# Performance work log

Measured on AMD Instinct MI355X. Metric: run time of the kernel, lower is better.

## Reference

```python
import jax, jax.numpy as jnp
import numpy as np

INPUT_SIZE = 16
HIDDEN = 256


def setup_inputs() -> dict:
    key = jax.random.key(0)
    ks = jax.random.split(key, 12)
    B, T, F, H = 512, 168, INPUT_SIZE, HIDDEN
    s_ih = 1.0 / np.sqrt(H)
    def u(k, shape):
        return jax.random.uniform(k, shape, jnp.float32, -s_ih, s_ih)
    return {
        "x": jax.random.normal(ks[0], (B, T, F), jnp.float32),
        # LSTM params, torch gate order (i, f, g, o) stacked along dim 0
        "w_ih": u(ks[1], (4 * H, F)),
        "w_hh": u(ks[2], (4 * H, H)),
        "b_ih": u(ks[3], (4 * H,)),
        "b_hh": u(ks[4], (4 * H,)),
        # MLP params
        "fc1_w": u(ks[5], (128, H)),
        "fc1_b": u(ks[6], (128,)),
        "fc2_w": u(ks[7], (64, 128)),
        "fc2_b": u(ks[8], (64,)),
        "fc3_w": u(ks[9], (1, 64)),
        "fc3_b": u(ks[10], (1,)),
    }


def _lstm(x, w_ih, w_hh, b_ih, b_hh):
    B, T, F = x.shape
    H = w_hh.shape[1]
    # Precompute input contribution for all timesteps: [B, T, 4H]
    x_proj = jnp.einsum("btf,gf->btg", x, w_ih) + b_ih + b_hh

    def step(carry, xp_t):
        h, c = carry
        gates = xp_t + h @ w_hh.T  # [B, 4H]
        i, f, g, o = jnp.split(gates, 4, axis=-1)
        i = jax.nn.sigmoid(i)
        f = jax.nn.sigmoid(f)
        g = jnp.tanh(g)
        o = jax.nn.sigmoid(o)
        c = f * c + i * g
        h = o * jnp.tanh(c)
        return (h, c), h

    h0 = jnp.zeros((B, H), x.dtype)
    c0 = jnp.zeros((B, H), x.dtype)
    (_, _), hs = jax.lax.scan(step, (h0, c0), jnp.swapaxes(x_proj, 0, 1))
    return jnp.swapaxes(hs, 0, 1)  # [B, T, H]


def reference(x, w_ih, w_hh, b_ih, b_hh, fc1_w, fc1_b, fc2_w, fc2_b, fc3_w, fc3_b):
    h = _lstm(x, w_ih, w_hh, b_ih, b_hh)          # [B, T, H]
    h = jax.nn.relu(h @ fc1_w.T + fc1_b)           # [B, T, 128]
    h = jax.nn.relu(h @ fc2_w.T + fc2_b)           # [B, T, 64]
    out = h @ fc3_w.T + fc3_b                      # [B, T, 1]
    return out
```

## Files before the change

### kernel.cpp

```cpp
#include <hip/hip_runtime.h>

typedef _Float16 half8 __attribute__((ext_vector_type(8)));
typedef float floatx4 __attribute__((ext_vector_type(4)));
typedef unsigned uint4v __attribute__((ext_vector_type(4)));

#define Bsz 512
#define Tsz 168
#define Fsz 16
#define Hsz 256
#define KTILES 9
#define LDS_K 296

#define WSW_OFF   0
#define BIAS_OFF  589824
#define HH_OFF    675840
#define XBUF_OFF  (HH_OFF + 44040192)

__global__ __launch_bounds__(256) void k_prep(
    const float* __restrict__ w_hh, const float* __restrict__ w_ih,
    const float* __restrict__ b_ih, const float* __restrict__ b_hh,
    _Float16* __restrict__ wsw, float* __restrict__ bias) {
    const int b = blockIdx.x, tid = threadIdx.x;
    const int lane = tid & 63, sub = tid >> 6;
    if (b < 144) {
        int tile = b * 4 + sub;
        int nt = tile / KTILES, kt = tile - nt * KTILES;
        int n_in = lane & 15, kg = lane >> 4;
        int J = nt >> 2, g = nt & 3;
        int n_orig = g * 256 + J * 16 + n_in;
        half8 v;
#pragma unroll
        for (int e = 0; e < 8; ++e) {
            int k = kt * 32 + kg * 8 + e;
            float f;
            if (k < 256)      f = w_hh[n_orig * 256 + k];
            else if (k < 272) f = w_ih[n_orig * 16 + (k - 256)];
            else              f = 0.0f;
            v[e] = (_Float16)f;
        }
        ((half8*)wsw)[tile * 64 + lane] = v;
    } else {
        int id = (b - 144) * 256 + tid;
        int nt = id >> 4, n = id & 15;
        int J = nt >> 2, g = nt & 3;
        int n_orig = g * 256 + J * 16 + n;
        bias[id] = b_ih[n_orig] + b_hh[n_orig];
    }
}

#define WG_BARRIER()                                          \
    do {                                                      \
        asm volatile("s_waitcnt lgkmcnt(0)" ::: "memory");    \
        __builtin_amdgcn_s_barrier();                         \
        __builtin_amdgcn_sched_barrier(0);                    \
    } while (0)

__global__ __launch_bounds__(512, 1) void k_lstm21(
    const float* __restrict__ x, const _Float16* __restrict__ wsw,
    const float* __restrict__ bias, unsigned* __restrict__ hh32,
    unsigned long long* __restrict__ xbuf) {
    __shared__ __align__(16) _Float16 h_lds[16][LDS_K];
    __shared__ float glds[4][16][68];

    const int tid = threadIdx.x;
    const int wave = tid >> 6, lane = tid & 63;
    const int n_in = lane & 15, quad = lane >> 4;
    const int bb = blockIdx.x & 31, ng = blockIdx.x >> 5;
    const int b0 = bb * 16;
    const int Jl = wave & 3;
    const int gp = wave >> 2;

    float bs[2];
    half8 wf[2][KTILES];
#pragma unroll
    for (int gg = 0; gg < 2; ++gg) {
        const int nt = ng * 16 + Jl * 4 + gp * 2 + gg;
        bs[gg] = bias[nt * 16 + n_in];
#pragma unroll
        for (int kt = 0; kt < KTILES; ++kt)
            wf[gg][kt] = ((const half8*)wsw)[((size_t)nt * KTILES + kt) * 64 + lane];
    }

    for (int i = tid; i < 16 * LDS_K; i += 512)
        ((_Float16*)h_lds)[i] = (_Float16)0.0f;
    __syncthreads();
    if (tid < 256) {
        int m = tid >> 4, f = tid & 15;
        h_lds[m][Hsz + f] = (_Float16)x[((b0 + m) * Tsz + 0) * Fsz + f];
    }
    __syncthreads();

    const int cm = tid >> 5, cj = tid & 31;
    float c_st[2] = {0.f, 0.f};

    for (int t = 0; t < Tsz; ++t) {
        half8 afr[KTILES];
#pragma unroll
        for (int kt = 0; kt < KTILES; ++kt)
            afr[kt] = *(const half8*)&h_lds[n_in][kt * 32 + quad * 8];

        floatx4 acc[2] = {(floatx4){0.f,0.f,0.f,0.f}, (floatx4){0.f,0.f,0.f,0.f}};
#pragma unroll
        for (int gg = 0; gg < 2; ++gg) {
#pragma unroll
            for (int kt = 0; kt < KTILES; ++kt)
                acc[gg] = __builtin_amdgcn_mfma_f32_16x16x32_f16(afr[kt], wf[gg][kt], acc[gg], 0, 0, 0);
        }

#pragma unroll
        for (int gg = 0; gg < 2; ++gg)
#pragma unroll
            for (int r = 0; r < 4; ++r)
                glds[gp * 2 + gg][quad * 4 + r][Jl * 16 + n_in] = acc[gg][r] + bs[gg];
        WG_BARRIER();

        union { _Float16 f[2]; unsigned u; } pk;
#pragma unroll
        for (int e = 0; e < 2; ++e) {
            int jl = 2 * cj + e;
            float ig = glds[0][cm][jl];
            float fg = glds[1][cm][jl];
            float gg_ = glds[2][cm][jl];
            float og = glds[3][cm][jl];
            float si = 1.0f / (1.0f + __expf(-ig));
            float sf = 1.0f / (1.0f + __expf(-fg));
            float tg = 1.0f - 2.0f / (__expf(2.0f * gg_) + 1.0f);
            float so = 1.0f / (1.0f + __expf(-og));
            float c = sf * c_st[e] + si * tg;
            c_st[e] = c;
            float th = 1.0f - 2.0f / (__expf(2.0f * c) + 1.0f);
            pk.f[e] = (_Float16)(so * th);
        }
        *(unsigned*)&h_lds[cm][ng * 64 + 2 * cj] = pk.u;

        const size_t rb = ((size_t)((bb * 2 + (t & 1)) * 16));
        if (t + 1 < Tsz) {
            unsigned long long pv = ((unsigned long long)pk.u << 32) | (unsigned)(t + 1);
            __hip_atomic_store(&xbuf[(rb + cm) * 128 + ng * 32 + cj], pv,
                               __ATOMIC_RELAXED, __HIP_MEMORY_SCOPE_AGENT);
        }
        __builtin_nontemporal_store(
            pk.u, &hh32[((size_t)(b0 + cm) * Tsz + t) * 128 + ng * 32 + cj]);

        if (t + 1 < Tsz) {
            float xr = 0.0f;
            if (tid < 256)
                xr = x[((b0 + (tid >> 4)) * Tsz + (t + 1)) * Fsz + (tid & 15)];

            const unsigned want = (unsigned)(t + 1);
            unsigned long long* p1 = &xbuf[(rb + cm) * 128 + ((ng + 1) & 3) * 32 + cj];
            unsigned long long* p2 = &xbuf[(rb + cm) * 128 + ((ng + 2) & 3) * 32 + cj];
            unsigned long long* p3 = &xbuf[(rb + cm) * 128 + ((ng + 3) & 3) * 32 + cj];
            unsigned long long v1 = __hip_atomic_load(p1, __ATOMIC_RELAXED,
                                                      __HIP_MEMORY_SCOPE_AGENT);
            unsigned long long v2 = __hip_atomic_load(p2, __ATOMIC_RELAXED,
                                                      __HIP_MEMORY_SCOPE_AGENT);
            unsigned long long v3 = __hip_atomic_load(p3, __ATOMIC_RELAXED,
                                                      __HIP_MEMORY_SCOPE_AGENT);
            while ((unsigned)v1 != want || (unsigned)v2 != want || (unsigned)v3 != want) {
                if ((unsigned)v1 != want)
                    v1 = __hip_atomic_load(p1, __ATOMIC_RELAXED, __HIP_MEMORY_SCOPE_AGENT);
                if ((unsigned)v2 != want)
                    v2 = __hip_atomic_load(p2, __ATOMIC_RELAXED, __HIP_MEMORY_SCOPE_AGENT);
                if ((unsigned)v3 != want)
                    v3 = __hip_atomic_load(p3, __ATOMIC_RELAXED, __HIP_MEMORY_SCOPE_AGENT);
            }
            *(unsigned*)&h_lds[cm][((ng + 1) & 3) * 64 + 2 * cj] = (unsigned)(v1 >> 32);
            *(unsigned*)&h_lds[cm][((ng + 2) & 3) * 64 + 2 * cj] = (unsigned)(v2 >> 32);
            *(unsigned*)&h_lds[cm][((ng + 3) & 3) * 64 + 2 * cj] = (unsigned)(v3 >> 32);
            if (tid < 256)
                h_lds[tid >> 4][Hsz + (tid & 15)] = (_Float16)xr;
            WG_BARRIER();
        }
    }
}

__global__ __launch_bounds__(512, 2) void k_mlp7(
    const _Float16* __restrict__ hh, const float* __restrict__ fc1_w,
    const float* __restrict__ fc2_w, const float* __restrict__ b1,
    const float* __restrict__ b2, const float* __restrict__ w3,
    const float* __restrict__ b3, float* __restrict__ out) {
    __shared__ __align__(16) _Float16 w1sh[64 * 512];
    __shared__ __align__(16) _Float16 w2sh[16 * 512];
    __shared__ _Float16 st1[8][16][136];
    __shared__ _Float16 st2[8][16][72];

    const int tid = threadIdx.x;
    const int wave = tid >> 6, lane = tid & 63;
    const int n_in = lane & 15, quad = lane >> 4;

    {
#pragma unroll
        for (int it = 0; it < 8; ++it) {
            int s = it * 512 + tid;
            int tile = s >> 6, ln = s & 63;
            int nt = tile >> 3, kt = tile & 7, ni = ln & 15, kg = ln >> 4;
            const float* src = &fc1_w[(nt * 16 + ni) * 256 + kt * 32 + kg * 8];
            half8 v;
#pragma unroll
            for (int e = 0; e < 8; ++e) v[e] = (_Float16)src[e];
            ((half8*)w1sh)[s] = v;
        }
#pragma unroll
        for (int it = 0; it < 2; ++it) {
            int s = it * 512 + tid;
            int tile = s >> 6, ln = s & 63;
            int nt = tile >> 2, kt = tile & 3, ni = ln & 15, kg = ln >> 4;
            const float* src = &fc2_w[(nt * 16 + ni) * 128 + kt * 32 + kg * 8];
            half8 v;
#pragma unroll
            for (int e = 0; e < 8; ++e) v[e] = (_Float16)src[e];
            ((half8*)w2sh)[s] = v;
        }
    }
    __syncthreads();

    uint4v bufA[8], bufB[8], bufC[8];
    const int ch0 = blockIdx.x, ch1 = blockIdx.x + 224, ch2 = blockIdx.x + 448;

#define MLP_LOAD(dst, ch)                                                      \
    {                                                                          \
        const int tok0_ = (ch) * 128 + wave * 16;                              \
        _Pragma("unroll")                                                      \
        for (int kt = 0; kt < 8; ++kt)                                         \
            dst[kt] = *(const uint4v*)&hh[(size_t)(tok0_ + n_in) * 256 +       \
                                          kt * 32 + quad * 8];                 \
    }

    MLP_LOAD(bufA, ch0)
    MLP_LOAD(bufB, ch1)
    MLP_LOAD(bufC, ch2)

    auto compute = [&](const uint4v* raw, int chunk) {
        const int tok0 = chunk * 128 + wave * 16;
        half8 afr[8];
#pragma unroll
        for (int kt = 0; kt < 8; ++kt)
            afr[kt] = __builtin_bit_cast(half8, raw[kt]);

#pragma unroll
        for (int nt = 0; nt < 8; ++nt) {
            floatx4 a = (floatx4){0.f, 0.f, 0.f, 0.f};
#pragma unroll
            for (int kt = 0; kt < 8; ++kt) {
                half8 bfr = *(const half8*)&w1sh[(nt * 8 + kt) * 512 + lane * 8];
                a = __builtin_amdgcn_mfma_f32_16x16x32_f16(afr[kt], bfr, a, 0, 0, 0);
            }
            float bbv = b1[nt * 16 + n_in];
#pragma unroll
            for (int r = 0; r < 4; ++r) {
                float v = a[r] + bbv;
                st1[wave][quad * 4 + r][nt * 16 + n_in] = (_Float16)(v > 0.f ? v : 0.f);
            }
        }

        half8 a2[4];
#pragma unroll
        for (int kt = 0; kt < 4; ++kt)
            a2[kt] = *(const half8*)&st1[wave][n_in][kt * 32 + quad * 8];
#pragma unroll
        for (int nt = 0; nt < 4; ++nt) {
            floatx4 a = (floatx4){0.f, 0.f, 0.f, 0.f};
#pragma unroll
            for (int kt = 0; kt < 4; ++kt) {
                half8 bfr = *(const half8*)&w2sh[(nt * 4 + kt) * 512 + lane * 8];
                a = __builtin_amdgcn_mfma_f32_16x16x32_f16(a2[kt], bfr, a, 0, 0, 0);
            }
            float bbv = b2[nt * 16 + n_in];
#pragma unroll
            for (int r = 0; r < 4; ++r) {
                float v = a[r] + bbv;
                st2[wave][quad * 4 + r][nt * 16 + n_in] = (_Float16)(v > 0.f ? v : 0.f);
            }
        }

        float p = 0.0f;
#pragma unroll
        for (int e = 0; e < 16; ++e)
            p += (float)st2[wave][n_in][quad * 16 + e] * w3[quad * 16 + e];
        p += __shfl_down(p, 32);
        p += __shfl_down(p, 16);
        if (quad == 0) out[tok0 + n_in] = p + b3[0];
    };

    compute(bufA, ch0);
    compute(bufB, ch1);
    compute(bufC, ch2);
#undef MLP_LOAD
}

extern "C" void kernel_launch(void* const* d_in, const int* in_sizes, int n_in,
                              void* d_out, int out_size, void* d_ws, size_t ws_size,
                              hipStream_t stream) {
    const float* x     = (const float*)d_in[0];
    const float* w_ih  = (const float*)d_in[1];
    const float* w_hh  = (const float*)d_in[2];
    const float* b_ih  = (const float*)d_in[3];
    const float* b_hh  = (const float*)d_in[4];
    const float* fc1_w = (const float*)d_in[5];
    const float* fc1_b = (const float*)d_in[6];
    const float* fc2_w = (const float*)d_in[7];
    const float* fc2_b = (const float*)d_in[8];
    const float* fc3_w = (const float*)d_in[9];
    const float* fc3_b = (const float*)d_in[10];

    char* ws = (char*)d_ws;
    _Float16* wsw  = (_Float16*)(ws + WSW_OFF);
    float*    bias = (float*)(ws + BIAS_OFF);
    _Float16* hhist= (_Float16*)(ws + HH_OFF);
    unsigned long long* xbuf = (unsigned long long*)(ws + XBUF_OFF);

    k_prep<<<148, 256, 0, stream>>>(w_hh, w_ih, b_ih, b_hh, wsw, bias);
    k_lstm21<<<128, 512, 0, stream>>>(x, wsw, bias, (unsigned*)hhist, xbuf);
    k_mlp7<<<224, 512, 0, stream>>>(hhist, fc1_w, fc2_w, fc1_b, fc2_b,
                                    fc3_w, fc3_b, (float*)d_out);
}
```

Before: 431.1 us.

## Overlap cross-block h exchange with local-slice MFMAs in LSTM recurrence

Each step now first runs the MFMAs over the block's own h slice and the x tile, then waits for the other three blocks' h slices, and only then finishes the remaining K tiles. The spin-wait on the exchange buffer moves to the start of the next step, with the first atomic loads issued at the end of the previous step, and the x row is prefetched one step ahead. Only 6 of the 18 weight fragments stay in registers. The other 12 are reloaded from global/L2 every step, which adds memory traffic inside the critical loop in exchange for lower register pressure and more overlap.

```diff
diff --git a/kernel.cpp b/kernel.cpp
--- a/kernel.cpp
+++ b/kernel.cpp
@@ -55,7 +55,7 @@
         __builtin_amdgcn_sched_barrier(0);                    \
     } while (0)
 
-__global__ __launch_bounds__(512, 1) void k_lstm21(
+__global__ __launch_bounds__(512, 1) void k_lstm22(
     const float* __restrict__ x, const _Float16* __restrict__ wsw,
     const float* __restrict__ bias, unsigned* __restrict__ hh32,
     unsigned long long* __restrict__ xbuf) {
@@ -70,16 +70,20 @@
     const int Jl = wave & 3;
     const int gp = wave >> 2;
 
+    const int nt0 = ng * 16 + Jl * 4 + gp * 2 + 0;
+    const int nt1 = ng * 16 + Jl * 4 + gp * 2 + 1;
+    const int kt_o0 = 2 * ng, kt_o1 = 2 * ng + 1;
+
     float bs[2];
-    half8 wf[2][KTILES];
-#pragma unroll
-    for (int gg = 0; gg < 2; ++gg) {
-        const int nt = ng * 16 + Jl * 4 + gp * 2 + gg;
-        bs[gg] = bias[nt * 16 + n_in];
-#pragma unroll
-        for (int kt = 0; kt < KTILES; ++kt)
-            wf[gg][kt] = ((const half8*)wsw)[((size_t)nt * KTILES + kt) * 64 + lane];
-    }
+    bs[0] = bias[nt0 * 16 + n_in];
+    bs[1] = bias[nt1 * 16 + n_in];
+    const half8* wsw8 = (const half8*)wsw;
+    half8 w0o0 = wsw8[((size_t)nt0 * KTILES + kt_o0) * 64 + lane];
+    half8 w0o1 = wsw8[((size_t)nt0 * KTILES + kt_o1) * 64 + lane];
+    half8 w0x  = wsw8[((size_t)nt0 * KTILES + 8) * 64 + lane];
+    half8 w1o0 = wsw8[((size_t)nt1 * KTILES + kt_o0) * 64 + lane];
+    half8 w1o1 = wsw8[((size_t)nt1 * KTILES + kt_o1) * 64 + lane];
+    half8 w1x  = wsw8[((size_t)nt1 * KTILES + 8) * 64 + lane];
 
     for (int i = tid; i < 16 * LDS_K; i += 512)
         ((_Float16*)h_lds)[i] = (_Float16)0.0f;
@@ -92,19 +96,53 @@
 
     const int cm = tid >> 5, cj = tid & 31;
     float c_st[2] = {0.f, 0.f};
+    unsigned long long pv1 = 0, pv2 = 0, pv3 = 0;
+    float xr_a = 0.f, xr_b = 0.f;
+    if (tid < 256 && 1 < Tsz)
+        xr_a = x[((b0 + (tid >> 4)) * Tsz + 1) * Fsz + (tid & 15)];
 
     for (int t = 0; t < Tsz; ++t) {
-        half8 afr[KTILES];
-#pragma unroll
-        for (int kt = 0; kt < KTILES; ++kt)
-            afr[kt] = *(const half8*)&h_lds[n_in][kt * 32 + quad * 8];
-
         floatx4 acc[2] = {(floatx4){0.f,0.f,0.f,0.f}, (floatx4){0.f,0.f,0.f,0.f}};
-#pragma unroll
-        for (int gg = 0; gg < 2; ++gg) {
-#pragma unroll
-            for (int kt = 0; kt < KTILES; ++kt)
-                acc[gg] = __builtin_amdgcn_mfma_f32_16x16x32_f16(afr[kt], wf[gg][kt], acc[gg], 0, 0, 0);
+        {
+            half8 a0 = *(const half8*)&h_lds[n_in][kt_o0 * 32 + quad * 8];
+            half8 a1 = *(const half8*)&h_lds[n_in][kt_o1 * 32 + quad * 8];
+            half8 ax = *(const half8*)&h_lds[n_in][8 * 32 + quad * 8];
+            acc[0] = __builtin_amdgcn_mfma_f32_16x16x32_f16(a0, w0o0, acc[0], 0, 0, 0);
+            acc[1] = __builtin_amdgcn_mfma_f32_16x16x32_f16(a0, w1o0, acc[1], 0, 0, 0);
+            acc[0] = __builtin_amdgcn_mfma_f32_16x16x32_f16(a1, w0o1, acc[0], 0, 0, 0);
+            acc[1] = __builtin_amdgcn_mfma_f32_16x16x32_f16(a1, w1o1, acc[1], 0, 0, 0);
+            acc[0] = __builtin_amdgcn_mfma_f32_16x16x32_f16(ax, w0x, acc[0], 0, 0, 0);
+            acc[1] = __builtin_amdgcn_mfma_f32_16x16x32_f16(ax, w1x, acc[1], 0, 0, 0);
+        }
+
+        if (t > 0) {
+            const unsigned want = (unsigned)t;
+            const size_t rbp = (size_t)((bb * 2 + ((t + 1) & 1)) * 16);
+            unsigned long long* p1 = &xbuf[(rbp + cm) * 128 + ((ng + 1) & 3) * 32 + cj];
+            unsigned long long* p2 = &xbuf[(rbp + cm) * 128 + ((ng + 2) & 3) * 32 + cj];
+            unsigned long long* p3 = &xbuf[(rbp + cm) * 128 + ((ng + 3) & 3) * 32 + cj];
+            while ((unsigned)pv1 != want || (unsigned)pv2 != want || (unsigned)pv3 != want) {
+                if ((unsigned)pv1 != want)
+                    pv1 = __hip_atomic_load(p1, __ATOMIC_RELAXED, __HIP_MEMORY_SCOPE_AGENT);
+                if ((unsigned)pv2 != want)
+                    pv2 = __hip_atomic_load(p2, __ATOMIC_RELAXED, __HIP_MEMORY_SCOPE_AGENT);
+                if ((unsigned)pv3 != want)
+                    pv3 = __hip_atomic_load(p3, __ATOMIC_RELAXED, __HIP_MEMORY_SCOPE_AGENT);
+            }
+            *(unsigned*)&h_lds[cm][((ng + 1) & 3) * 64 + 2 * cj] = (unsigned)(pv1 >> 32);
+            *(unsigned*)&h_lds[cm][((ng + 2) & 3) * 64 + 2 * cj] = (unsigned)(pv2 >> 32);
+            *(unsigned*)&h_lds[cm][((ng + 3) & 3) * 64 + 2 * cj] = (unsigned)(pv3 >> 32);
+        }
+        WG_BARRIER();
+
+#pragma unroll
+        for (int i = 0; i < 6; ++i) {
+            const int kt = (kt_o0 + 2 + i) & 7;
+            half8 a  = *(const half8*)&h_lds[n_in][kt * 32 + quad * 8];
+            half8 wA = wsw8[((size_t)nt0 * KTILES + kt) * 64 + lane];
+            half8 wB = wsw8[((size_t)nt1 * KTILES + kt) * 64 + lane];
+            acc[0] = __builtin_amdgcn_mfma_f32_16x16x32_f16(a, wA, acc[0], 0, 0, 0);
+            acc[1] = __builtin_amdgcn_mfma_f32_16x16x32_f16(a, wB, acc[1], 0, 0, 0);
         }
 
 #pragma unroll
@@ -143,34 +181,19 @@
             pk.u, &hh32[((size_t)(b0 + cm) * Tsz + t) * 128 + ng * 32 + cj]);
 
         if (t + 1 < Tsz) {
-            float xr = 0.0f;
+            pv1 = __hip_atomic_load(&xbuf[(rb + cm) * 128 + ((ng + 1) & 3) * 32 + cj],
+                                    __ATOMIC_RELAXED, __HIP_MEMORY_SCOPE_AGENT);
+            pv2 = __hip_atomic_load(&xbuf[(rb + cm) * 128 + ((ng + 2) & 3) * 32 + cj],
+                                    __ATOMIC_RELAXED, __HIP_MEMORY_SCOPE_AGENT);
+            pv3 = __hip_atomic_load(&xbuf[(rb + cm) * 128 + ((ng + 3) & 3) * 32 + cj],
+                                    __ATOMIC_RELAXED, __HIP_MEMORY_SCOPE_AGENT);
+            if (t + 2 < Tsz && tid < 256)
+                xr_b = x[((b0 + (tid >> 4)) * Tsz + (t + 2)) * Fsz + (tid & 15)];
+
             if (tid < 256)
-                xr = x[((b0 + (tid >> 4)) * Tsz + (t + 1)) * Fsz + (tid & 15)];
-
-            const unsigned want = (unsigned)(t + 1);
-            unsigned long long* p1 = &xbuf[(rb + cm) * 128 + ((ng + 1) & 3) * 32 + cj];
-            unsigned long long* p2 = &xbuf[(rb + cm) * 128 + ((ng + 2) & 3) * 32 + cj];
-            unsigned long long* p3 = &xbuf[(rb + cm) * 128 + ((ng + 3) & 3) * 32 + cj];
-            unsigned long long v1 = __hip_atomic_load(p1, __ATOMIC_RELAXED,
-                                                      __HIP_MEMORY_SCOPE_AGENT);
-            unsigned long long v2 = __hip_atomic_load(p2, __ATOMIC_RELAXED,
-                                                      __HIP_MEMORY_SCOPE_AGENT);
-            unsigned long long v3 = __hip_atomic_load(p3, __ATOMIC_RELAXED,
-                                                      __HIP_MEMORY_SCOPE_AGENT);
-            while ((unsigned)v1 != want || (unsigned)v2 != want || (unsigned)v3 != want) {
-                if ((unsigned)v1 != want)
-                    v1 = __hip_atomic_load(p1, __ATOMIC_RELAXED, __HIP_MEMORY_SCOPE_AGENT);
-                if ((unsigned)v2 != want)
-                    v2 = __hip_atomic_load(p2, __ATOMIC_RELAXED, __HIP_MEMORY_SCOPE_AGENT);
-                if ((unsigned)v3 != want)
-                    v3 = __hip_atomic_load(p3, __ATOMIC_RELAXED, __HIP_MEMORY_SCOPE_AGENT);
-            }
-            *(unsigned*)&h_lds[cm][((ng + 1) & 3) * 64 + 2 * cj] = (unsigned)(v1 >> 32);
-            *(unsigned*)&h_lds[cm][((ng + 2) & 3) * 64 + 2 * cj] = (unsigned)(v2 >> 32);
-            *(unsigned*)&h_lds[cm][((ng + 3) & 3) * 64 + 2 * cj] = (unsigned)(v3 >> 32);
-            if (tid < 256)
-                h_lds[tid >> 4][Hsz + (tid & 15)] = (_Float16)xr;
+                h_lds[tid >> 4][Hsz + (tid & 15)] = (_Float16)xr_a;
             WG_BARRIER();
+            xr_a = xr_b;
         }
     }
 }
@@ -311,7 +334,7 @@
     unsigned long long* xbuf = (unsigned long long*)(ws + XBUF_OFF);
 
     k_prep<<<148, 256, 0, stream>>>(w_hh, w_ih, b_ih, b_hh, wsw, bias);
-    k_lstm21<<<128, 512, 0, stream>>>(x, wsw, bias, (unsigned*)hhist, xbuf);
+    k_lstm22<<<128, 512, 0, stream>>>(x, wsw, bias, (unsigned*)hhist, xbuf);
     k_mlp7<<<224, 512, 0, stream>>>(hhist, fc1_w, fc2_w, fc1_b, fc2_b,
                                     fc3_w, fc3_b, (float*)d_out);
 }
```

After: 590.1 us. 36.9% more time.
